# Kernel tuning notes

Measured on AMD Instinct MI355X. Metric: run time of the kernel, lower is better.

The kernel has to match this reference:

```python
import jax, jax.numpy as jnp
import numpy as np

LN_EPS = 1e-5

def setup_inputs() -> dict:
    key = jax.random.key(0)
    ks = jax.random.split(key, 16)
    B, N = 16384, 1000000
    return {
        "user_input": jax.random.randint(ks[0], (B,), 0, N),
        "emb": jax.random.normal(ks[1], (N, 64), jnp.float32),
        "sc_country_idx": jax.random.randint(ks[2], (N,), 0, 256),
        "sc_country_emb": jax.random.normal(ks[3], (256, 32), jnp.float32),
        "sc_device_idx": jax.random.randint(ks[4], (N,), 0, 10000),
        "sc_device_emb": jax.random.normal(ks[5], (10000, 32), jnp.float32),
        "mf_tags_idx": jax.random.randint(ks[6], (N, 20), 0, 50000),
        "mf_tags_emb": jax.random.normal(ks[7], (50000, 32), jnp.float32),
        "mf_history_idx": jax.random.randint(ks[8], (N, 50), 0, 100000),
        "mf_history_emb": jax.random.normal(ks[9], (100000, 32), jnp.float32),
        "fc_w": jax.random.normal(ks[10], (256, 192), jnp.float32) * 0.05,
        "fc_b": jax.random.normal(ks[11], (256,), jnp.float32) * 0.05,
        "ln_g": jnp.ones((256,), jnp.float32),
        "ln_b": jnp.zeros((256,), jnp.float32),
    }

def _layernorm(x, g, b):
    mu = jnp.mean(x, axis=-1, keepdims=True)
    var = jnp.mean(jnp.square(x - mu), axis=-1, keepdims=True)
    return (x - mu) * jax.lax.rsqrt(var + LN_EPS) * g + b

def reference(user_input, emb, sc_country_idx, sc_country_emb, sc_device_idx, sc_device_emb,
               mf_tags_idx, mf_tags_emb, mf_history_idx, mf_history_emb,
               fc_w, fc_b, ln_g, ln_b):
    parts = [emb[user_input]]  # [B, 64]
    # scalar side features: buffer lookup then embedding gather -> [B, 32]
    parts.append(sc_country_emb[sc_country_idx[user_input]])
    parts.append(sc_device_emb[sc_device_idx[user_input]])
    # multi-valued side features: [B, W] index lists -> gather -> mean pool -> [B, 32]
    parts.append(jnp.mean(mf_tags_emb[mf_tags_idx[user_input]], axis=1))
    parts.append(jnp.mean(mf_history_emb[mf_history_idx[user_input]], axis=1))
    x = jnp.concatenate(parts, axis=-1)  # [B, 192]
    x = jax.nn.relu(x @ fc_w.T + fc_b)   # [B, 256]
    return _layernorm(x, ln_g, ln_b)
```

## Files before the change

kernel.cpp:

```cpp
#include <hip/hip_runtime.h>

#define LN_EPS 1e-5f

constexpr int ROWS_PER_BLOCK = 32;
constexpr int ROWS_PER_WAVE  = 8;
constexpr int KDIM = 192;
constexpr int NOUT = 256;

__global__ __launch_bounds__(256)
void user_tower_kernel(const int*   __restrict__ user_input,
                       const float* __restrict__ emb,
                       const int*   __restrict__ sc_country_idx,
                       const float* __restrict__ sc_country_emb,
                       const int*   __restrict__ sc_device_idx,
                       const float* __restrict__ sc_device_emb,
                       const int*   __restrict__ mf_tags_idx,
                       const float* __restrict__ mf_tags_emb,
                       const int*   __restrict__ mf_history_idx,
                       const float* __restrict__ mf_history_emb,
                       const float* __restrict__ fc_w,
                       const float* __restrict__ fc_b,
                       const float* __restrict__ ln_g,
                       const float* __restrict__ ln_b,
                       float*       __restrict__ out,
                       int B)
{
    __shared__ float X[ROWS_PER_BLOCK][KDIM];

    const int tid  = threadIdx.x;
    const int lane = tid & 63;
    const int wave = tid >> 6;
    const int row0 = blockIdx.x * ROWS_PER_BLOCK;

    const int half = lane >> 5;
    const int col  = lane & 31;

    for (int i = 0; i < ROWS_PER_WAVE; ++i) {
        const int r   = wave * ROWS_PER_WAVE + i;
        const int row = row0 + r;
        if (row < B) {
            const int u = __builtin_amdgcn_readfirstlane(user_input[row]);

            X[r][lane] = emb[u * 64 + lane];

            if (half == 0) {
                const int ci = sc_country_idx[u];
                X[r][64 + col] = sc_country_emb[ci * 32 + col];
            } else {
                const int di = sc_device_idx[u];
                X[r][96 + col] = sc_device_emb[di * 32 + col];
            }

            {
                float a = 0.f;
                const int* __restrict__ ip = mf_tags_idx + u * 20;
                #pragma unroll
                for (int j = 0; j < 20; j += 2) {
                    const int idx = ip[j + half];
                    a += mf_tags_emb[idx * 32 + col];
                }
                a += __shfl_xor(a, 32, 64);
                if (half == 0) X[r][128 + col] = a * (1.f / 20.f);
            }

            {
                float a = 0.f;
                const int* __restrict__ ip = mf_history_idx + u * 50;
                #pragma unroll
                for (int j = 0; j < 50; j += 2) {
                    const int idx = ip[j + half];
                    a += mf_history_emb[idx * 32 + col];
                }
                a += __shfl_xor(a, 32, 64);
                if (half == 0) X[r][160 + col] = a * (1.f / 50.f);
            }
        }
    }
    __syncthreads();

    const int c0 = lane;
    float acc[ROWS_PER_WAVE][4];
    float g4[4], b4[4];
    #pragma unroll
    for (int ci = 0; ci < 4; ++ci) {
        const int c = c0 + 64 * ci;
        const float bias = fc_b[c];
        g4[ci] = ln_g[c];
        b4[ci] = ln_b[c];
        #pragma unroll
        for (int ri = 0; ri < ROWS_PER_WAVE; ++ri) acc[ri][ci] = bias;
    }

    for (int kc = 0; kc < KDIM; kc += 4) {
        float4 w[4];
        #pragma unroll
        for (int ci = 0; ci < 4; ++ci)
            w[ci] = *(const float4*)&fc_w[(c0 + 64 * ci) * KDIM + kc];
        #pragma unroll
        for (int ri = 0; ri < ROWS_PER_WAVE; ++ri) {
            const float4 x = *(const float4*)&X[wave * ROWS_PER_WAVE + ri][kc];
            #pragma unroll
            for (int ci = 0; ci < 4; ++ci) {
                acc[ri][ci] += x.x * w[ci].x + x.y * w[ci].y
                             + x.z * w[ci].z + x.w * w[ci].w;
            }
        }
    }

    #pragma unroll
    for (int ri = 0; ri < ROWS_PER_WAVE; ++ri) {
        const int row = row0 + wave * ROWS_PER_WAVE + ri;
        float y[4];
        float s = 0.f, s2 = 0.f;
        #pragma unroll
        for (int ci = 0; ci < 4; ++ci) {
            y[ci] = fmaxf(acc[ri][ci], 0.f);
            s  += y[ci];
            s2 += y[ci] * y[ci];
        }
        #pragma unroll
        for (int m = 32; m >= 1; m >>= 1) {
            s  += __shfl_xor(s,  m, 64);
            s2 += __shfl_xor(s2, m, 64);
        }
        const float mu  = s  * (1.f / 256.f);
        const float var = s2 * (1.f / 256.f) - mu * mu;
        const float rs  = rsqrtf(var + LN_EPS);
        if (row < B) {
            #pragma unroll
            for (int ci = 0; ci < 4; ++ci) {
                const int c = c0 + 64 * ci;
                out[row * NOUT + c] = (y[ci] - mu) * rs * g4[ci] + b4[ci];
            }
        }
    }
}

extern "C" void kernel_launch(void* const* d_in, const int* in_sizes, int n_in,
                              void* d_out, int out_size, void* d_ws, size_t ws_size,
                              hipStream_t stream)
{
    const int*   user_input     = (const int*)  d_in[0];
    const float* emb            = (const float*)d_in[1];
    const int*   sc_country_idx = (const int*)  d_in[2];
    const float* sc_country_emb = (const float*)d_in[3];
    const int*   sc_device_idx  = (const int*)  d_in[4];
    const float* sc_device_emb  = (const float*)d_in[5];
    const int*   mf_tags_idx    = (const int*)  d_in[6];
    const float* mf_tags_emb    = (const float*)d_in[7];
    const int*   mf_history_idx = (const int*)  d_in[8];
    const float* mf_history_emb = (const float*)d_in[9];
    const float* fc_w           = (const float*)d_in[10];
    const float* fc_b           = (const float*)d_in[11];
    const float* ln_g           = (const float*)d_in[12];
    const float* ln_b           = (const float*)d_in[13];
    float*       out            = (float*)d_out;

    const int B = in_sizes[0];
    const int grid = (B + ROWS_PER_BLOCK - 1) / ROWS_PER_BLOCK;

    user_tower_kernel<<<grid, 256, 0, stream>>>(
        user_input, emb, sc_country_idx, sc_country_emb,
        sc_device_idx, sc_device_emb, mf_tags_idx, mf_tags_emb,
        mf_history_idx, mf_history_emb, fc_w, fc_b, ln_g, ln_b, out, B);
}
```

Measured before the change: 529.7 us.

## Split gather into separate high-occupancy kernel writing X to workspace

The fused kernel is split in two. The first kernel performs the embedding gathers with one wave per row and preloads all index lists into registers so the gathers can be issued with more memory-level parallelism. The second kernel loads X from workspace into shared memory and runs the FC, ReLU and LayerNorm as before. This targets latency-bound serial gathers, at the cost of an extra global round-trip of X (B×192 floats) and a second launch.

```diff
diff --git a/kernel.cpp b/kernel.cpp
--- a/kernel.cpp
+++ b/kernel.cpp
@@ -2,28 +2,81 @@
 
 #define LN_EPS 1e-5f
 
+constexpr int KDIM = 192;
+constexpr int NOUT = 256;
 constexpr int ROWS_PER_BLOCK = 32;
 constexpr int ROWS_PER_WAVE  = 8;
-constexpr int KDIM = 192;
-constexpr int NOUT = 256;
 
 __global__ __launch_bounds__(256)
-void user_tower_kernel(const int*   __restrict__ user_input,
-                       const float* __restrict__ emb,
-                       const int*   __restrict__ sc_country_idx,
-                       const float* __restrict__ sc_country_emb,
-                       const int*   __restrict__ sc_device_idx,
-                       const float* __restrict__ sc_device_emb,
-                       const int*   __restrict__ mf_tags_idx,
-                       const float* __restrict__ mf_tags_emb,
-                       const int*   __restrict__ mf_history_idx,
-                       const float* __restrict__ mf_history_emb,
-                       const float* __restrict__ fc_w,
-                       const float* __restrict__ fc_b,
-                       const float* __restrict__ ln_g,
-                       const float* __restrict__ ln_b,
-                       float*       __restrict__ out,
-                       int B)
+void ut_gather_kernel(const int*   __restrict__ user_input,
+                      const float* __restrict__ emb,
+                      const int*   __restrict__ sc_country_idx,
+                      const float* __restrict__ sc_country_emb,
+                      const int*   __restrict__ sc_device_idx,
+                      const float* __restrict__ sc_device_emb,
+                      const int*   __restrict__ mf_tags_idx,
+                      const float* __restrict__ mf_tags_emb,
+                      const int*   __restrict__ mf_history_idx,
+                      const float* __restrict__ mf_history_emb,
+                      float*       __restrict__ X,
+                      int B)
+{
+    const int lane = threadIdx.x & 63;
+    const int wave = threadIdx.x >> 6;
+    const int row  = blockIdx.x * 4 + wave;
+    if (row >= B) return;
+
+    const int half = lane >> 5;
+    const int col  = lane & 31;
+
+    const int u = __builtin_amdgcn_readfirstlane(user_input[row]);
+    float* __restrict__ Xr = X + (size_t)row * KDIM;
+
+    const int ci = sc_country_idx[u];
+    const int di = sc_device_idx[u];
+
+    const int* __restrict__ tp = mf_tags_idx    + (size_t)u * 20;
+    const int* __restrict__ hp = mf_history_idx + (size_t)u * 50;
+    int tix[10];
+    #pragma unroll
+    for (int j = 0; j < 10; ++j) tix[j] = tp[2 * j + half];
+    int hix[25];
+    #pragma unroll
+    for (int j = 0; j < 25; ++j) hix[j] = hp[2 * j + half];
+
+    const float e = emb[(size_t)u * 64 + lane];
+
+    const float sc = (half == 0) ? sc_country_emb[ci * 32 + col]
+                                 : sc_device_emb [di * 32 + col];
+
+    float ta = 0.f;
+    #pragma unroll
+    for (int j = 0; j < 10; ++j) ta += mf_tags_emb[tix[j] * 32 + col];
+    float ha = 0.f;
+    #pragma unroll
+    for (int j = 0; j < 25; ++j) ha += mf_history_emb[hix[j] * 32 + col];
+
+    ta += __shfl_xor(ta, 32, 64);
+    ha += __shfl_xor(ha, 32, 64);
+
+    Xr[lane] = e;
+    if (half == 0) {
+        Xr[64  + col] = sc;
+        Xr[128 + col] = ta * (1.f / 20.f);
+        Xr[160 + col] = ha * (1.f / 50.f);
+    } else {
+        Xr[96  + col] = sc;
+    }
+}
+
+__global__ __launch_bounds__(256)
+void ut_fc_ln_kernel(const float* __restrict__ Xg,
+                     const float* __restrict__ fc_w,
+                     const float* __restrict__ fc_b,
+                     const float* __restrict__ ln_g,
+                     const float* __restrict__ ln_b,
+                     float*       __restrict__ out,
+                     int B)
 {
     __shared__ float X[ROWS_PER_BLOCK][KDIM];
 
@@ -32,49 +85,11 @@
     const int wave = tid >> 6;
     const int row0 = blockIdx.x * ROWS_PER_BLOCK;
 
-    const int half = lane >> 5;
-    const int col  = lane & 31;
-
-    for (int i = 0; i < ROWS_PER_WAVE; ++i) {
-        const int r   = wave * ROWS_PER_WAVE + i;
-        const int row = row0 + r;
-        if (row < B) {
-            const int u = __builtin_amdgcn_readfirstlane(user_input[row]);
-
-            X[r][lane] = emb[u * 64 + lane];
-
-            if (half == 0) {
-                const int ci = sc_country_idx[u];
-                X[r][64 + col] = sc_country_emb[ci * 32 + col];
-            } else {
-                const int di = sc_device_idx[u];
-                X[r][96 + col] = sc_device_emb[di * 32 + col];
-            }
-
-            {
-                float a = 0.f;
-                const int* __restrict__ ip = mf_tags_idx + u * 20;
-                #pragma unroll
-                for (int j = 0; j < 20; j += 2) {
-                    const int idx = ip[j + half];
-                    a += mf_tags_emb[idx * 32 + col];
-                }
-                a += __shfl_xor(a, 32, 64);
-                if (half == 0) X[r][128 + col] = a * (1.f / 20.f);
-            }
-
-            {
-                float a = 0.f;
-                const int* __restrict__ ip = mf_history_idx + u * 50;
-                #pragma unroll
-                for (int j = 0; j < 50; j += 2) {
-                    const int idx = ip[j + half];
-                    a += mf_history_emb[idx * 32 + col];
-                }
-                a += __shfl_xor(a, 32, 64);
-                if (half == 0) X[r][160 + col] = a * (1.f / 50.f);
-            }
-        }
+    {
+        const float4* __restrict__ src = (const float4*)(Xg + (size_t)row0 * KDIM);
+        float4* dst = (float4*)&X[0][0];
+        #pragma unroll
+        for (int i = 0; i < 6; ++i) dst[tid + 256 * i] = src[tid + 256 * i];
     }
     __syncthreads();
 
@@ -155,12 +170,17 @@
     const float* ln_g           = (const float*)d_in[12];
     const float* ln_b           = (const float*)d_in[13];
     float*       out            = (float*)d_out;
+    float*       X              = (float*)d_ws;
 
     const int B = in_sizes[0];
-    const int grid = (B + ROWS_PER_BLOCK - 1) / ROWS_PER_BLOCK;
 
-    user_tower_kernel<<<grid, 256, 0, stream>>>(
+    const int gatherGrid = (B + 3) / 4;
+    ut_gather_kernel<<<gatherGrid, 256, 0, stream>>>(
         user_input, emb, sc_country_idx, sc_country_emb,
         sc_device_idx, sc_device_emb, mf_tags_idx, mf_tags_emb,
-        mf_history_idx, mf_history_emb, fc_w, fc_b, ln_g, ln_b, out, B);
+        mf_history_idx, mf_history_emb, X, B);
+
+    const int fcGrid = (B + ROWS_PER_BLOCK - 1) / ROWS_PER_BLOCK;
+    ut_fc_ln_kernel<<<fcGrid, 256, 0, stream>>>(
+        X, fc_w, fc_b, ln_g, ln_b, out, B);
 }
```

Result: faster. 516.5 us (-2.5%).
